# Kernel tuning notes

Hardware: AMD Instinct MI355X
Metric: run time of the kernel (lower is better)

Reference implementation:

```python
import jax, jax.numpy as jnp
import numpy as np
from jax import lax

B, C, H, W = 8, 128, 96, 96
EXPAN = 4           # expan_att_chans
NUM_CHANS = 2
NUM_HEADS = NUM_CHANS * EXPAN          # 8
HEAD_DIM = C * EXPAN // NUM_HEADS      # 64
EPS = 1e-12  # F.normalize eps


def _gconv(x, w, b, groups):
    # torch Conv2d(kernel=3, padding=1, groups=groups), OIHW weight layout
    y = lax.conv_general_dilated(x, w, (1, 1), 'SAME',
                                 feature_group_count=groups,
                                 dimension_numbers=('NCHW', 'OIHW', 'NCHW'))
    return y + b[None, :, None, None]


def setup_inputs() -> dict:
    key = jax.random.key(0)
    k0, k1, k2 = jax.random.split(key, 3)
    x = jax.random.normal(k0, (B, C, H, W), jnp.float32)
    w_qkv = jax.random.normal(k1, (C * EXPAN * 3, 1, 3, 3), jnp.float32) * 0.05
    b_qkv = jnp.zeros((C * EXPAN * 3,), jnp.float32)
    t = jnp.ones((1, NUM_HEADS, 1, 1), jnp.float32)
    w_fus = jax.random.normal(k2, (C, EXPAN, 3, 3), jnp.float32) * 0.05
    b_fus = jnp.zeros((C,), jnp.float32)
    return {"x": x, "w_qkv": w_qkv, "b_qkv": b_qkv, "t": t,
            "w_fus": w_fus, "b_fus": b_fus}


def reference(x, w_qkv, b_qkv, t, w_fus, b_fus):
    # depthwise-grouped qkv conv: [B, C*EXPAN*3, H, W]
    qkv = _gconv(x, w_qkv, b_qkv, C)
    # view(B, C, 3e, H, W).transpose(1,2) -> [B, 3e, C, H, W]
    qkv = qkv.reshape(B, C, 3 * EXPAN, H, W).transpose(0, 2, 1, 3, 4)
    q, k, v = jnp.split(qkv, 3, axis=1)  # each [B, EXPAN, C, H, W]

    def heads(a):
        return a.reshape(B, NUM_HEADS, HEAD_DIM, H * W)

    q, k, v = heads(q), heads(k), heads(v)

    def l2n(a):
        return a / jnp.maximum(jnp.linalg.norm(a, axis=-1, keepdims=True), EPS)

    q, k = l2n(q), l2n(k)
    attn = jnp.einsum('bhdn,bhen->bhde', q, k) * t   # [B, nh, hd, hd]
    attn = jax.nn.softmax(attn, axis=-1)
    o = jnp.einsum('bhde,bhen->bhdn', attn, v)       # [B, nh, hd, HW]
    # view(B, EXPAN, C, H, W).transpose(1,2).flatten(1,2) -> [B, C*EXPAN, H, W]
    o = o.reshape(B, EXPAN, C, H, W).transpose(0, 2, 1, 3, 4).reshape(B, C * EXPAN, H, W)
    return _gconv(o, w_fus, b_fus, C)
```

## Files before the change

kernel.cpp:

```cpp
#include <hip/hip_runtime.h>
#include <hip/hip_bf16.h>
#include <stdint.h>

#define BB     8
#define CC     128
#define HW     9216
#define NHEAD  8
#define HD     64
#define NCH    16
#define CHUNK  576

typedef __hip_bfloat16 bf16;
using frag16 = __attribute__((ext_vector_type(8))) short;
using f32x4  = __attribute__((ext_vector_type(4))) float;

__device__ __forceinline__ float b2f(bf16 v) { return __bfloat162float(v); }
__device__ __forceinline__ bf16  f2b(float v) { return __float2bfloat16(v); }

__device__ __forceinline__ float us2f(unsigned short u) {
  union { unsigned int i; float f; } c; c.i = ((unsigned int)u) << 16; return c.f;
}

__device__ __forceinline__ unsigned int pack2(float a, float b) {
  union { __hip_bfloat162 h2; unsigned int u; } c;
  c.h2 = __float22bfloat162_rn(make_float2(a, b));
  return c.u;
}

__global__ __launch_bounds__(256) void k1_qkv(
    const float* __restrict__ x, const float* __restrict__ wq,
    const float* __restrict__ bq,
    bf16* __restrict__ qg, bf16* __restrict__ kg, bf16* __restrict__ vg,
    float* __restrict__ qn2, float* __restrict__ kn2) {
  __shared__ float xs[98 * 100 + 4];
  __shared__ float red[32];
  int tid = threadIdx.x;
  int wave = tid >> 6, lane = tid & 63;
  int b = blockIdx.x >> 7, c = blockIdx.x & 127;
  const float* xp = x + (size_t)(b * CC + c) * HW;
  for (int i = tid; i < (98 * 100 + 4) / 4; i += 256)
    ((float4*)xs)[i] = make_float4(0.f, 0.f, 0.f, 0.f);
  __syncthreads();
  for (int i = tid; i < 96 * 24; i += 256) {
    int y = i / 24, g4 = i - y * 24;
    ((float4*)(xs + (y + 1) * 100 + 4))[g4] = ((const float4*)(xp + y * 96))[g4];
  }
  __syncthreads();

  int half = c >> 6, d = c & 63;
  int nidx[8];
  size_t basep[12];
#pragma unroll
  for (int j = 0; j < 12; ++j) {
    int e = j & 3;
    int h = e * 2 + half;
    int ni = (b * NHEAD + h) * HD + d;
    if (j < 8) nidx[j] = ni;
    basep[j] = (size_t)ni * HW;
  }
  const float* wrow = wq + c * 108;
  const float* brow = bq + c * 12;

  float ssq[8];
#pragma unroll
  for (int j = 0; j < 8; ++j) ssq[j] = 0.f;

#pragma unroll 1
  for (int it = 0; it < 5; ++it) {
    int u = it * 256 + tid;
    if (u < 1152) {
      int ly = u / 12;
      int x8 = (u - ly * 12) * 8;
      int p0 = ly * 96 + x8;
      float w10[3][10];
#pragma unroll
      for (int ky = 0; ky < 3; ++ky) {
        int basea = (ly + ky) * 100 + 4 + x8;
        float4 M0 = *(const float4*)&xs[basea];
        float4 M1 = *(const float4*)&xs[basea + 4];
        w10[ky][0] = xs[basea - 1];
        w10[ky][1] = M0.x; w10[ky][2] = M0.y; w10[ky][3] = M0.z; w10[ky][4] = M0.w;
        w10[ky][5] = M1.x; w10[ky][6] = M1.y; w10[ky][7] = M1.z; w10[ky][8] = M1.w;
        w10[ky][9] = xs[basea + 8];
      }
#pragma unroll
      for (int j = 0; j < 12; ++j) {
        float bias = brow[j];
        float a[8];
#pragma unroll
        for (int p = 0; p < 8; ++p) a[p] = bias;
#pragma unroll
        for (int ky = 0; ky < 3; ++ky)
#pragma unroll
          for (int kx = 0; kx < 3; ++kx) {
            float w = wrow[j * 9 + ky * 3 + kx];
#pragma unroll
            for (int p = 0; p < 8; ++p)
              a[p] = fmaf(w, w10[ky][kx + p], a[p]);
          }
        uint4 st;
        st.x = pack2(a[0], a[1]); st.y = pack2(a[2], a[3]);
        st.z = pack2(a[4], a[5]); st.w = pack2(a[6], a[7]);
        if (j < 4)      *(uint4*)(qg + basep[j] + p0) = st;
        else if (j < 8) *(uint4*)(kg + basep[j] + p0) = st;
        else            *(uint4*)(vg + basep[j] + p0) = st;
        if (j < 8) {
          float s2 = 0.f;
#pragma unroll
          for (int p = 0; p < 8; ++p) s2 = fmaf(a[p], a[p], s2);
          ssq[j] += s2;
        }
      }
    }
  }
#pragma unroll
  for (int j = 0; j < 8; ++j) {
    float v = ssq[j];
#pragma unroll
    for (int off = 32; off > 0; off >>= 1) v += __shfl_down(v, off);
    if (lane == 0) red[wave * 8 + j] = v;
  }
  __syncthreads();
  if (tid < 8) {
    float s = red[tid] + red[8 + tid] + red[16 + tid] + red[24 + tid];
    if (tid < 4) qn2[nidx[tid]] = s;
    else         kn2[nidx[tid]] = s;
  }
}

__global__ __launch_bounds__(256) void k2_gram(
    const bf16* __restrict__ qg, const bf16* __restrict__ kg,
    float* __restrict__ part) {
  int tid = threadIdx.x;
  int wave = tid >> 6;
  int lane = tid & 63;
  int chunk = blockIdx.x;
  int bh = blockIdx.y;
  const size_t base = (size_t)bh * HD * HW;
  int m = lane & 15;
  int k8 = (lane >> 4) * 8;
  const bf16* qrow  = qg + base + (size_t)(wave * 16 + m) * HW + k8;
  const bf16* krow0 = kg + base + (size_t)m * HW + k8;
  f32x4 acc0 = {0.f, 0.f, 0.f, 0.f}, acc1 = acc0, acc2 = acc0, acc3 = acc0;
  for (int kb = 0; kb < CHUNK; kb += 32) {
    int off = chunk * CHUNK + kb;
    frag16 a  = *(const frag16*)(qrow + off);
    frag16 b0 = *(const frag16*)(krow0 + off);
    frag16 b1 = *(const frag16*)(krow0 + (size_t)16 * HW + off);
    frag16 b2 = *(const frag16*)(krow0 + (size_t)32 * HW + off);
    frag16 b3 = *(const frag16*)(krow0 + (size_t)48 * HW + off);
    acc0 = __builtin_amdgcn_mfma_f32_16x16x32_bf16(a, b0, acc0, 0, 0, 0);
    acc1 = __builtin_amdgcn_mfma_f32_16x16x32_bf16(a, b1, acc1, 0, 0, 0);
    acc2 = __builtin_amdgcn_mfma_f32_16x16x32_bf16(a, b2, acc2, 0, 0, 0);
    acc3 = __builtin_amdgcn_mfma_f32_16x16x32_bf16(a, b3, acc3, 0, 0, 0);
  }
  float* po = part + (size_t)(bh * NCH + chunk) * 4096;
  int dr = wave * 16 + (lane >> 4) * 4;
  int e0 = lane & 15;
#pragma unroll
  for (int r = 0; r < 4; ++r) {
    po[(dr + r) * 64 +  0 + e0] = acc0[r];
    po[(dr + r) * 64 + 16 + e0] = acc1[r];
    po[(dr + r) * 64 + 32 + e0] = acc2[r];
    po[(dr + r) * 64 + 48 + e0] = acc3[r];
  }
}

__global__ __launch_bounds__(256) void k2_softmax(
    const float* __restrict__ part, bf16* __restrict__ ah, bf16* __restrict__ al,
    const float* __restrict__ qn2, const float* __restrict__ kn2,
    const float* __restrict__ t_f) {
  __shared__ float kns[64];
  int bh = blockIdx.x;
  int dq = blockIdx.y;
  int tid = threadIdx.x;
  if (tid < 64) kns[tid] = fmaxf(sqrtf(kn2[bh * 64 + tid]), 1e-12f);
  __syncthreads();
  int d  = dq * 16 + (tid >> 4);
  int e0 = (tid & 15) * 4;

  const float* pb = part + (size_t)bh * NCH * 4096 + d * 64 + e0;
  float4 s = make_float4(0.f, 0.f, 0.f, 0.f);
#pragma unroll
  for (int ch = 0; ch < NCH; ++ch) {
    float4 g = *(const float4*)&pb[ch * 4096];
    s.x += g.x; s.y += g.y; s.z += g.z; s.w += g.w;
  }
  float v[4] = {s.x, s.y, s.z, s.w};
  float sc = t_f[bh & 7] / fmaxf(sqrtf(qn2[bh * 64 + d]), 1e-12f);
  float m = -1e30f;
#pragma unroll
  for (int j = 0; j < 4; ++j) {
    v[j] = v[j] * sc / kns[e0 + j];
    m = fmaxf(m, v[j]);
  }
  m = fmaxf(m, __shfl_xor(m, 1));
  m = fmaxf(m, __shfl_xor(m, 2));
  m = fmaxf(m, __shfl_xor(m, 4));
  m = fmaxf(m, __shfl_xor(m, 8));
  float ssum = 0.f;
#pragma unroll
  for (int j = 0; j < 4; ++j) { v[j] = __expf(v[j] - m); ssum += v[j]; }
  ssum += __shfl_xor(ssum, 1);
  ssum += __shfl_xor(ssum, 2);
  ssum += __shfl_xor(ssum, 4);
  ssum += __shfl_xor(ssum, 8);
  float inv = 1.f / ssum;
  unsigned short hi16[4], lo16[4];
#pragma unroll
  for (int j = 0; j < 4; ++j) {
    float p = v[j] * inv;
    bf16 hi = f2b(p);
    float lo = p - b2f(hi);
    bf16 lov = f2b(lo);
    hi16[j] = *(unsigned short*)&hi;
    lo16[j] = *(unsigned short*)&lov;
  }
  const size_t base = (size_t)bh * 4096 + d * 64 + e0;
  *(ushort4*)(ah + base) = *(ushort4*)&hi16[0];
  *(ushort4*)(al + base) = *(ushort4*)&lo16[0];
}

__global__ __launch_bounds__(256) void k3_av(
    const bf16* __restrict__ ah, const bf16* __restrict__ al,
    const bf16* __restrict__ vg, bf16* __restrict__ og) {
  int tid = threadIdx.x;
  int wave = tid >> 6, lane = tid & 63;
  int chunk = blockIdx.x;
  int bh = blockIdx.y;
  int b = bh >> 3, h = bh & 7;
  int n0 = chunk * 256;
  int m = lane & 15;
  int k8 = (lane >> 4) * 8;
  int nwbase = wave * 64;

  const bf16* ahp = ah + (size_t)bh * 4096;
  const bf16* alp = al + (size_t)bh * 4096;
  frag16 a_hi[4][2], a_lo[4][2];
#pragma unroll
  for (int dt = 0; dt < 4; ++dt)
#pragma unroll
    for (int kh = 0; kh < 2; ++kh) {
      a_hi[dt][kh] = *(const frag16*)(ahp + (dt * 16 + m) * 64 + kh * 32 + k8);
      a_lo[dt][kh] = *(const frag16*)(alp + (dt * 16 + m) * 64 + kh * 32 + k8);
    }

  const bf16* vb = vg + (size_t)bh * HD * HW + n0 + nwbase + m;
  frag16 bfr[4][2];
#pragma unroll
  for (int kh = 0; kh < 2; ++kh)
#pragma unroll
    for (int j = 0; j < 8; ++j) {
      const bf16* vp = vb + (size_t)(kh * 32 + k8 + j) * HW;
      bfr[0][kh][j] = *(const short*)(vp);
      bfr[1][kh][j] = *(const short*)(vp + 16);
      bfr[2][kh][j] = *(const short*)(vp + 32);
      bfr[3][kh][j] = *(const short*)(vp + 48);
    }

  f32x4 acc[4][4];
#pragma unroll
  for (int dt = 0; dt < 4; ++dt)
#pragma unroll
    for (int nt = 0; nt < 4; ++nt) acc[dt][nt] = {0.f, 0.f, 0.f, 0.f};

#pragma unroll
  for (int nt = 0; nt < 4; ++nt)
#pragma unroll
    for (int kh = 0; kh < 2; ++kh)
#pragma unroll
      for (int dt = 0; dt < 4; ++dt) {
        acc[dt][nt] = __builtin_amdgcn_mfma_f32_16x16x32_bf16(a_hi[dt][kh], bfr[nt][kh], acc[dt][nt], 0, 0, 0);
        acc[dt][nt] = __builtin_amdgcn_mfma_f32_16x16x32_bf16(a_lo[dt][kh], bfr[nt][kh], acc[dt][nt], 0, 0, 0);
      }

  int cc0 = (h & 1) * 256 + (h >> 1);
  bf16* ob = og + (size_t)b * 512 * HW;
  int q4 = (lane >> 4) * 4;
#pragma unroll
  for (int dt = 0; dt < 4; ++dt)
#pragma unroll
    for (int nt = 0; nt < 4; ++nt) {
      int n = n0 + nwbase + nt * 16 + m;
#pragma unroll
      for (int r = 0; r < 4; ++r) {
        int d = dt * 16 + q4 + r;
        ob[(size_t)(cc0 + d * 4) * HW + n] = f2b(acc[dt][nt][r]);
      }
    }
}

__global__ __launch_bounds__(256) void k4_fuse(
    const bf16* __restrict__ og, const float* __restrict__ wf,
    const float* __restrict__ bfu, float* __restrict__ out) {
  __shared__ float lds[26 * 100 * 4];
  int tid = threadIdx.x;
  int tile = blockIdx.x;
  int bc = blockIdx.y;
  int b = bc >> 7, c = bc & 127;
  for (int i = tid; i < (26 * 100 * 4) / 4; i += 256)
    ((float4*)lds)[i] = make_float4(0.f, 0.f, 0.f, 0.f);
  __syncthreads();
  int r0 = tile * 24 - 1;
  const bf16* op = og + (size_t)(b * 512 + c * 4) * HW;
  for (int i = tid; i < 26 * 24; i += 256) {
    int rr = i / 24, g4 = i - rr * 24;
    int gr = r0 + rr;
    if (gr >= 0 && gr < 96) {
      int gp = gr * 96 + g4 * 4;
      ushort4 p0 = *(const ushort4*)(op + gp);
      ushort4 p1 = *(const ushort4*)(op + HW + gp);
      ushort4 p2 = *(const ushort4*)(op + 2 * HW + gp);
      ushort4 p3 = *(const ushort4*)(op + (size_t)3 * HW + gp);
      float* dst = &lds[(rr * 100 + 2 + g4 * 4) * 4];
      *(float4*)(dst +  0) = make_float4(us2f(p0.x), us2f(p1.x), us2f(p2.x), us2f(p3.x));
      *(float4*)(dst +  4) = make_float4(us2f(p0.y), us2f(p1.y), us2f(p2.y), us2f(p3.y));
      *(float4*)(dst +  8) = make_float4(us2f(p0.z), us2f(p1.z), us2f(p2.z), us2f(p3.z));
      *(float4*)(dst + 12) = make_float4(us2f(p0.w), us2f(p1.w), us2f(p2.w), us2f(p3.w));
    }
  }
  __syncthreads();
  const float* wrow = wf + c * 36;
  float bias = bfu[c];
  float* outp = out + (size_t)(b * CC + c) * HW + tile * 24 * 96;
#pragma unroll
  for (int pi = 0; pi < 9; ++pi) {
    int p = pi * 256 + tid;
    int ry = p / 96, x = p - ry * 96;
    float a0 = bias, a1 = 0.f, a2 = 0.f, a3 = 0.f;
#pragma unroll
    for (int ky = 0; ky < 3; ++ky)
#pragma unroll
      for (int kx = 0; kx < 3; ++kx) {
        const float4 vv = *(const float4*)&lds[((ry + ky) * 100 + 1 + x + kx) * 4];
        a0 = fmaf(wrow[0 + ky * 3 + kx],  vv.x, a0);
        a1 = fmaf(wrow[9 + ky * 3 + kx],  vv.y, a1);
        a2 = fmaf(wrow[18 + ky * 3 + kx], vv.z, a2);
        a3 = fmaf(wrow[27 + ky * 3 + kx], vv.w, a3);
      }
    outp[p] = (a0 + a1) + (a2 + a3);
  }
}

extern "C" void kernel_launch(void* const* d_in, const int* in_sizes, int n_in,
                              void* d_out, int out_size, void* d_ws, size_t ws_size,
                              hipStream_t stream) {
  (void)in_sizes; (void)n_in; (void)out_size; (void)ws_size;
  const float* x   = (const float*)d_in[0];
  const float* wq  = (const float*)d_in[1];
  const float* bq  = (const float*)d_in[2];
  const float* tt  = (const float*)d_in[3];
  const float* wf  = (const float*)d_in[4];
  const float* bfu = (const float*)d_in[5];

  char* ws = (char*)d_ws;
  bf16*  qg    = (bf16*)(ws + 0);
  bf16*  kg    = (bf16*)(ws + 75497472);
  bf16*  vg    = (bf16*)(ws + 150994944);
  float* part  = (float*)(ws + 226492416);
  bf16*  ah    = (bf16*)(ws + 243269632);
  bf16*  al    = (bf16*)(ws + 243793920);
  float* qn2   = (float*)(ws + 244318208);
  float* kn2   = (float*)(ws + 244334592);
  bf16*  og    = qg;
  float* out   = (float*)d_out;

  hipLaunchKernelGGL(k1_qkv, dim3(1024), dim3(256), 0, stream,
                     x, wq, bq, qg, kg, vg, qn2, kn2);
  hipLaunchKernelGGL(k2_gram, dim3(NCH, 64), dim3(256), 0, stream, qg, kg, part);
  hipLaunchKernelGGL(k2_softmax, dim3(64, 4), dim3(256), 0, stream,
                     part, ah, al, qn2, kn2, tt);
  hipLaunchKernelGGL(k3_av, dim3(36, 64), dim3(256), 0, stream, ah, al, vg, og);
  hipLaunchKernelGGL(k4_fuse, dim3(4, 1024), dim3(256), 0, stream, og, wf, bfu, out);
}
```

Before: 251.3 us.

## Stage gram-matrix tiles through double-buffered LDS and trim halo zeroing

The Q·K^T gram kernel now loads 64-column slabs of Q and K cooperatively into padded, double-buffered shared memory and feeds the MFMA fragments from LDS. The next slab's global loads are prefetched while the current one is computed. Before, each wave read its own scattered fragments straight from global memory with little overlap. The conv staging in k1 and k4 now zeroes only the halo border instead of the whole LDS tile, removing a full clear and one barrier. The price is extra LDS traffic and a barrier per slab in the gram kernel.

```diff
diff --git a/kernel.cpp b/kernel.cpp
--- a/kernel.cpp
+++ b/kernel.cpp
@@ -9,6 +9,7 @@
 #define HD     64
 #define NCH    16
 #define CHUNK  576
+#define KPAD   68
 
 typedef __hip_bfloat16 bf16;
 using frag16 = __attribute__((ext_vector_type(8))) short;
@@ -25,6 +26,29 @@
   union { __hip_bfloat162 h2; unsigned int u; } c;
   c.h2 = __float22bfloat162_rn(make_float2(a, b));
   return c.u;
+}
+
+__device__ __forceinline__ frag16 ldsfrag(const unsigned short* p) {
+  uint2 lo = *(const uint2*)p;
+  uint2 hi = *(const uint2*)(p + 4);
+  union { unsigned int u[4]; frag16 f; } c;
+  c.u[0] = lo.x; c.u[1] = lo.y; c.u[2] = hi.x; c.u[3] = hi.y;
+  return c.f;
+}
+__device__ __forceinline__ void ldsst(unsigned short* p, uint4 v) {
+  *(uint2*)p = make_uint2(v.x, v.y);
+  *(uint2*)(p + 4) = make_uint2(v.z, v.w);
+}
+
+__device__ __forceinline__ void stage_plane(float* xs, const float* xp, int tid) {
+  const float4 z4 = make_float4(0.f, 0.f, 0.f, 0.f);
+  for (int i = tid; i < 98; i += 256) *(float4*)&xs[i * 100] = z4;
+  for (int i = tid; i < 24; i += 256) *(float4*)&xs[4 + i * 4] = z4;
+  for (int i = tid; i < 25; i += 256) *(float4*)&xs[9704 + i * 4] = z4;
+  for (int i = tid; i < 96 * 24; i += 256) {
+    int y = i / 24, g4 = i - y * 24;
+    ((float4*)(xs + (y + 1) * 100 + 4))[g4] = ((const float4*)(xp + y * 96))[g4];
+  }
 }
 
 __global__ __launch_bounds__(256) void k1_qkv(
@@ -38,13 +62,7 @@
   int wave = tid >> 6, lane = tid & 63;
   int b = blockIdx.x >> 7, c = blockIdx.x & 127;
   const float* xp = x + (size_t)(b * CC + c) * HW;
-  for (int i = tid; i < (98 * 100 + 4) / 4; i += 256)
-    ((float4*)xs)[i] = make_float4(0.f, 0.f, 0.f, 0.f);
-  __syncthreads();
-  for (int i = tid; i < 96 * 24; i += 256) {
-    int y = i / 24, g4 = i - y * 24;
-    ((float4*)(xs + (y + 1) * 100 + 4))[g4] = ((const float4*)(xp + y * 96))[g4];
-  }
+  stage_plane(xs, xp, tid);
   __syncthreads();
 
   int half = c >> 6, d = c & 63;
@@ -131,29 +149,71 @@
 __global__ __launch_bounds__(256) void k2_gram(
     const bf16* __restrict__ qg, const bf16* __restrict__ kg,
     float* __restrict__ part) {
+  __shared__ unsigned short sq[2][64 * KPAD];
+  __shared__ unsigned short sk[2][64 * KPAD];
   int tid = threadIdx.x;
   int wave = tid >> 6;
   int lane = tid & 63;
   int chunk = blockIdx.x;
   int bh = blockIdx.y;
   const size_t base = (size_t)bh * HD * HW;
+  int n0 = chunk * CHUNK;
+
+  int srow = tid >> 3;
+  int sseg = tid & 7;
+  const bf16* qs0 = qg + base + (size_t)srow * HW + n0 + sseg * 8;
+  const bf16* qs1 = qs0 + (size_t)32 * HW;
+  const bf16* ks0 = kg + base + (size_t)srow * HW + n0 + sseg * 8;
+  const bf16* ks1 = ks0 + (size_t)32 * HW;
+  int d0 = srow * KPAD + sseg * 8;
+  int d1 = (srow + 32) * KPAD + sseg * 8;
+
   int m = lane & 15;
-  int k8 = (lane >> 4) * 8;
-  const bf16* qrow  = qg + base + (size_t)(wave * 16 + m) * HW + k8;
-  const bf16* krow0 = kg + base + (size_t)m * HW + k8;
+  int k8 = lane >> 4;
+  int arow = wave * 16 + m;
+
   f32x4 acc0 = {0.f, 0.f, 0.f, 0.f}, acc1 = acc0, acc2 = acc0, acc3 = acc0;
-  for (int kb = 0; kb < CHUNK; kb += 32) {
-    int off = chunk * CHUNK + kb;
-    frag16 a  = *(const frag16*)(qrow + off);
-    frag16 b0 = *(const frag16*)(krow0 + off);
-    frag16 b1 = *(const frag16*)(krow0 + (size_t)16 * HW + off);
-    frag16 b2 = *(const frag16*)(krow0 + (size_t)32 * HW + off);
-    frag16 b3 = *(const frag16*)(krow0 + (size_t)48 * HW + off);
-    acc0 = __builtin_amdgcn_mfma_f32_16x16x32_bf16(a, b0, acc0, 0, 0, 0);
-    acc1 = __builtin_amdgcn_mfma_f32_16x16x32_bf16(a, b1, acc1, 0, 0, 0);
-    acc2 = __builtin_amdgcn_mfma_f32_16x16x32_bf16(a, b2, acc2, 0, 0, 0);
-    acc3 = __builtin_amdgcn_mfma_f32_16x16x32_bf16(a, b3, acc3, 0, 0, 0);
-  }
+
+  uint4 rq0 = *(const uint4*)(qs0);
+  uint4 rq1 = *(const uint4*)(qs1);
+  uint4 rk0 = *(const uint4*)(ks0);
+  uint4 rk1 = *(const uint4*)(ks1);
+  ldsst(&sq[0][d0], rq0); ldsst(&sq[0][d1], rq1);
+  ldsst(&sk[0][d0], rk0); ldsst(&sk[0][d1], rk1);
+  __syncthreads();
+
+#pragma unroll 1
+  for (int s = 0; s < 9; ++s) {
+    if (s < 8) {
+      int off = (s + 1) * 64;
+      rq0 = *(const uint4*)(qs0 + off);
+      rq1 = *(const uint4*)(qs1 + off);
+      rk0 = *(const uint4*)(ks0 + off);
+      rk1 = *(const uint4*)(ks1 + off);
+    }
+    const unsigned short* sqc = sq[s & 1];
+    const unsigned short* skc = sk[s & 1];
+#pragma unroll
+    for (int kk = 0; kk < 2; ++kk) {
+      int co = kk * 32 + k8 * 8;
+      frag16 a  = ldsfrag(&sqc[arow * KPAD + co]);
+      frag16 b0 = ldsfrag(&skc[(m +  0) * KPAD + co]);
+      frag16 b1 = ldsfrag(&skc[(m + 16) * KPAD + co]);
+      frag16 b2 = ldsfrag(&skc[(m + 32) * KPAD + co]);
+      frag16 b3 = ldsfrag(&skc[(m + 48) * KPAD + co]);
+      acc0 = __builtin_amdgcn_mfma_f32_16x16x32_bf16(a, b0, acc0, 0, 0, 0);
+      acc1 = __builtin_amdgcn_mfma_f32_16x16x32_bf16(a, b1, acc1, 0, 0, 0);
+      acc2 = __builtin_amdgcn_mfma_f32_16x16x32_bf16(a, b2, acc2, 0, 0, 0);
+      acc3 = __builtin_amdgcn_mfma_f32_16x16x32_bf16(a, b3, acc3, 0, 0, 0);
+    }
+    if (s < 8) {
+      int nb = (s + 1) & 1;
+      ldsst(&sq[nb][d0], rq0); ldsst(&sq[nb][d1], rq1);
+      ldsst(&sk[nb][d0], rk0); ldsst(&sk[nb][d1], rk1);
+      __syncthreads();
+    }
+  }
+
   float* po = part + (size_t)(bh * NCH + chunk) * 4096;
   int dr = wave * 16 + (lane >> 4) * 4;
   int e0 = lane & 15;
@@ -298,10 +358,16 @@
   int tile = blockIdx.x;
   int bc = blockIdx.y;
   int b = bc >> 7, c = bc & 127;
-  for (int i = tid; i < (26 * 100 * 4) / 4; i += 256)
-    ((float4*)lds)[i] = make_float4(0.f, 0.f, 0.f, 0.f);
-  __syncthreads();
   int r0 = tile * 24 - 1;
+  const float4 z4 = make_float4(0.f, 0.f, 0.f, 0.f);
+  for (int i = tid; i < 52; i += 256) {
+    int rr = i >> 1, cc = (i & 1) ? 98 : 1;
+    *(float4*)&lds[(rr * 100 + cc) * 4] = z4;
+  }
+  if (r0 < 0)
+    for (int i = tid; i < 96; i += 256) *(float4*)&lds[(0 * 100 + 2 + i) * 4] = z4;
+  if (r0 + 25 >= 96)
+    for (int i = tid; i < 96; i += 256) *(float4*)&lds[(25 * 100 + 2 + i) * 4] = z4;
   const bf16* op = og + (size_t)(b * 512 + c * 4) * HW;
   for (int i = tid; i < 26 * 24; i += 256) {
     int rr = i / 24, g4 = i - rr * 24;
```

Measured after the change: 232.9 us. 7.4% less time.
